# Kernel tuning notes

Hardware: AMD Instinct MI355X
Metric: run time of the kernel (lower is better)

The kernel has to match this reference:

```python
import jax, jax.numpy as jnp
import numpy as np

B, N, D, K, H = 64, 4096, 256, 11, 512
ITERS = 5
EPS = 1e-8
LN_EPS = 1e-5  # torch LayerNorm default
SCALE = D ** -0.5


def _ln(x, w, b):
    m = jnp.mean(x, axis=-1, keepdims=True)
    v = jnp.mean(jnp.square(x - m), axis=-1, keepdims=True)
    return (x - m) * jax.lax.rsqrt(v + LN_EPS) * w + b


def setup_inputs() -> dict:
    key = jax.random.key(0)
    ks = jax.random.split(key, 16)
    s = lambda k, shp, fan: jax.random.normal(k, shp, jnp.float32) * (1.0 / np.sqrt(fan))
    return {
        "inputs": jax.random.normal(ks[0], (B, N, D), jnp.float32),
        "slots_init": jax.random.normal(ks[1], (B, K, D), jnp.float32),
        "ln_f_w": jnp.ones((D,), jnp.float32), "ln_f_b": jnp.zeros((D,), jnp.float32),
        "ln_s_w": jnp.ones((D,), jnp.float32), "ln_s_b": jnp.zeros((D,), jnp.float32),
        "ln_p_w": jnp.ones((D,), jnp.float32), "ln_p_b": jnp.zeros((D,), jnp.float32),
        "Wq": s(ks[2], (D, D), D),
        "Wk": s(ks[3], (D, D), D),
        "Wv": s(ks[4], (D, D), D),
        "W_ih": s(ks[5], (3 * D, D), D), "b_ih": jnp.zeros((3 * D,), jnp.float32),
        "W_hh": s(ks[6], (3 * D, D), D), "b_hh": jnp.zeros((3 * D,), jnp.float32),
        "W1": s(ks[7], (H, D), D), "b1": jnp.zeros((H,), jnp.float32),
        "W2": s(ks[8], (D, H), H), "b2": jnp.zeros((D,), jnp.float32),
    }


def reference(inputs, slots_init, ln_f_w, ln_f_b, ln_s_w, ln_s_b, ln_p_w, ln_p_b,
              Wq, Wk, Wv, W_ih, b_ih, W_hh, b_hh, W1, b1, W2, b2):
    x = _ln(inputs, ln_f_w, ln_f_b)              # (B, N, D)
    k = x @ Wk.T                                  # (B, N, D)
    v = x @ Wv.T                                  # (B, N, D)
    slots = slots_init                            # (B, K, D)
    for _ in range(ITERS):
        slots_prev = slots
        q = _ln(slots, ln_s_w, ln_s_b) @ Wq.T     # (B, K, D)
        dots = jnp.einsum('bid,bjd->bij', q, k) * SCALE  # (B, K, N)
        attn = jax.nn.softmax(dots, axis=1) + EPS        # softmax over slots
        attn = attn / jnp.sum(attn, axis=-1, keepdims=True)
        updates = jnp.einsum('bjd,bij->bid', v, attn)    # (B, K, D)
        # GRUCell (torch semantics)
        gi = updates @ W_ih.T + b_ih              # (B, K, 3D)
        gh = slots_prev @ W_hh.T + b_hh
        i_r, i_z, i_n = jnp.split(gi, 3, axis=-1)
        h_r, h_z, h_n = jnp.split(gh, 3, axis=-1)
        r = jax.nn.sigmoid(i_r + h_r)
        z = jax.nn.sigmoid(i_z + h_z)
        n_ = jnp.tanh(i_n + r * h_n)
        slots = (1.0 - z) * n_ + z * slots_prev
        # residual MLP
        p = _ln(slots, ln_p_w, ln_p_b)
        slots = slots + jnp.maximum(p @ W1.T + b1, 0.0) @ W2.T + b2
    return slots
```

## Files before the change

kernel.cpp:

```cpp
#include <hip/hip_runtime.h>

typedef __bf16 bf16_t;
typedef bf16_t bf16x8 __attribute__((ext_vector_type(8)));
typedef bf16_t bf16x4 __attribute__((ext_vector_type(4)));
typedef float f32x4 __attribute__((ext_vector_type(4)));

#define DEVI static __device__ __forceinline__

constexpr int BB = 64;
constexpr int NN = 4096;
constexpr int DD = 256;
constexpr int KS = 11;
constexpr int KP = 16;
constexpr int HH = 512;
constexpr float EPS_A = 1e-8f;
constexpr float LNEPS = 1e-5f;
constexpr float SCALE = 0.0625f;
constexpr int MR = BB * KP;

DEVI float wredf(float v) {
#pragma unroll
  for (int o = 32; o > 0; o >>= 1) v += __shfl_xor(v, o, 64);
  return v;
}

DEVI float sigm(float x) { return 1.f / (1.f + __expf(-x)); }

__global__ void prep_weights_k(
    const float* __restrict__ s0, const float* __restrict__ s1, const float* __restrict__ s2,
    const float* __restrict__ s3, const float* __restrict__ s4, const float* __restrict__ s5,
    const float* __restrict__ s6,
    bf16_t* d0, bf16_t* d1, bf16_t* d2, bf16_t* d3, bf16_t* d4, bf16_t* d5, bf16_t* d6) {
  int i = blockIdx.x * 256 + threadIdx.x;
  const float* s; bf16_t* d; int o;
  if      (i < 65536)  { s = s0; d = d0; o = i; }
  else if (i < 131072) { s = s1; d = d1; o = i - 65536; }
  else if (i < 196608) { s = s2; d = d2; o = i - 131072; }
  else if (i < 393216) { s = s3; d = d3; o = i - 196608; }
  else if (i < 589824) { s = s4; d = d4; o = i - 393216; }
  else if (i < 720896) { s = s5; d = d5; o = i - 589824; }
  else                 { s = s6; d = d6; o = i - 720896; }
  d[o] = (bf16_t)s[o];
}

__global__ void init_slots_k(const float* __restrict__ si, float* __restrict__ slots) {
  int i = blockIdx.x * 256 + threadIdx.x;
  int d = i & 255, row = i >> 8, b = row >> 4, k = row & 15;
  slots[i] = (k < KS) ? si[((long)b * KS + k) * DD + d] : 0.f;
}

__global__ void ln_inputs_k(const float* __restrict__ x, const float* __restrict__ w,
                            const float* __restrict__ bsk, bf16_t* __restrict__ o) {
  const int wvi = threadIdx.x >> 6, lane = threadIdx.x & 63;
  const long row = (long)blockIdx.x * 4 + wvi;
  const float4 v = ((const float4*)(x + row * DD))[lane];
  float s = v.x + v.y + v.z + v.w;
  float s2 = v.x * v.x + v.y * v.y + v.z * v.z + v.w * v.w;
  s = wredf(s); s2 = wredf(s2);
  const float mean = s * (1.f / DD);
  const float var = s2 * (1.f / DD) - mean * mean;
  const float rstd = rsqrtf(var + LNEPS);
  const float4 w4 = ((const float4*)w)[lane];
  const float4 b4 = ((const float4*)bsk)[lane];
  bf16x4 ov;
  ov[0] = (bf16_t)((v.x - mean) * rstd * w4.x + b4.x);
  ov[1] = (bf16_t)((v.y - mean) * rstd * w4.y + b4.y);
  ov[2] = (bf16_t)((v.z - mean) * rstd * w4.z + b4.z);
  ov[3] = (bf16_t)((v.w - mean) * rstd * w4.w + b4.w);
  ((bf16x4*)(o + row * DD))[lane] = ov;
}

template <int MODE>
__global__ __launch_bounds__(256) void gemm_big_k(const bf16_t* __restrict__ X,
                                                  const bf16_t* __restrict__ W,
                                                  bf16_t* __restrict__ out) {
  __shared__ bf16_t As[128 * 72];
  __shared__ bf16_t Bs[256 * 72];
  const bf16_t* Ap; const bf16_t* Bp;
  if (MODE == 0) { Ap = W + (long)blockIdx.y * 128 * DD; Bp = X + (long)blockIdx.x * 256 * DD; }
  else           { Ap = X + (long)blockIdx.x * 128 * DD; Bp = W; }
  const int tid = threadIdx.x;
  const int wvi = tid >> 6, lane = tid & 63;
  const int c = lane & 15, q = lane >> 4;
  const int mh = wvi >> 1, nh = wvi & 1;
  f32x4 acc[4][8];
#pragma unroll
  for (int a = 0; a < 4; a++)
#pragma unroll
    for (int b = 0; b < 8; b++) acc[a][b] = (f32x4){0.f, 0.f, 0.f, 0.f};
  for (int kb = 0; kb < DD; kb += 64) {
#pragma unroll
    for (int it = 0; it < 4; ++it) {
      int id = it * 256 + tid, r = id >> 3, ch = id & 7;
      *(bf16x8*)(As + r * 72 + ch * 8) = *(const bf16x8*)(Ap + (long)r * DD + kb + ch * 8);
    }
#pragma unroll
    for (int it = 0; it < 8; ++it) {
      int id = it * 256 + tid, r = id >> 3, ch = id & 7;
      *(bf16x8*)(Bs + r * 72 + ch * 8) = *(const bf16x8*)(Bp + (long)r * DD + kb + ch * 8);
    }
    __syncthreads();
#pragma unroll
    for (int ks = 0; ks < 2; ++ks) {
      bf16x8 af[4], bfr[8];
#pragma unroll
      for (int mt = 0; mt < 4; mt++)
        af[mt] = *(const bf16x8*)(As + (mh * 64 + mt * 16 + c) * 72 + ks * 32 + q * 8);
#pragma unroll
      for (int nt = 0; nt < 8; nt++)
        bfr[nt] = *(const bf16x8*)(Bs + (nh * 128 + nt * 16 + c) * 72 + ks * 32 + q * 8);
#pragma unroll
      for (int mt = 0; mt < 4; mt++)
#pragma unroll
        for (int nt = 0; nt < 8; nt++)
          acc[mt][nt] = __builtin_amdgcn_mfma_f32_16x16x32_bf16(af[mt], bfr[nt], acc[mt][nt], 0, 0, 0);
    }
    __syncthreads();
  }
#pragma unroll
  for (int mt = 0; mt < 4; mt++) {
#pragma unroll
    for (int nt = 0; nt < 8; nt++) {
      bf16x4 o;
#pragma unroll
      for (int r = 0; r < 4; r++) o[r] = (bf16_t)acc[mt][nt][r];
      if (MODE == 0) {
        int dg = blockIdx.y * 128 + mh * 64 + mt * 16 + q * 4;
        long ng = (long)blockIdx.x * 256 + nh * 128 + nt * 16 + c;
        *(bf16x4*)(out + ng * DD + dg) = o;
      } else {
        long ng = (long)blockIdx.x * 128 + mh * 64 + mt * 16 + q * 4;
        int d = nh * 128 + nt * 16 + c;
        long b = ng >> 12; int nin = (int)(ng & 4095);
        *(bf16x4*)(out + (b * DD + d) * NN + nin) = o;
      }
    }
  }
}

__global__ void ln_slots_k(const float* __restrict__ slots, const float* __restrict__ lw,
                           const float* __restrict__ lb, bf16_t* __restrict__ sln,
                           bf16_t* __restrict__ spl, float* __restrict__ upd_raw,
                           float* __restrict__ rowsum) {
  const int row = blockIdx.x, d = threadIdx.x;
  upd_raw[row * DD + d] = 0.f;
  if (row < 4) rowsum[row * 256 + d] = 0.f;
  const int kk = row & 15;
  const int idx = row * DD + d;
  if (kk >= KS) { sln[idx] = (bf16_t)0.f; spl[idx] = (bf16_t)0.f; return; }
  float v = slots[idx];
  spl[idx] = (bf16_t)v;
  __shared__ float r1[4], r2[4];
  float s = wredf(v), s2 = wredf(v * v);
  const int wvi = threadIdx.x >> 6, lane = threadIdx.x & 63;
  if (lane == 0) { r1[wvi] = s; r2[wvi] = s2; }
  __syncthreads();
  float mean = (r1[0] + r1[1] + r1[2] + r1[3]) * (1.f / DD);
  float var = (r2[0] + r2[1] + r2[2] + r2[3]) * (1.f / DD) - mean * mean;
  float rstd = rsqrtf(var + LNEPS);
  sln[idx] = (bf16_t)((v - mean) * rstd * lw[d] + lb[d]);
}

template <bool BIASF, bool RELUF, bool RESF, int OUTM>
__global__ void small_gemm_k(const bf16_t* __restrict__ A, const bf16_t* __restrict__ W,
                             const float* __restrict__ bias, const float* __restrict__ res,
                             void* __restrict__ out, int C, int Kd) {
  const int lane = threadIdx.x & 63, c = lane & 15, q = lane >> 4;
  const int wid = blockIdx.x * 4 + (threadIdx.x >> 6);
  const int nct = C >> 4;
  const int mt = wid / nct, ct = wid % nct;
  const bf16_t* ap = A + (long)(mt * 16 + c) * Kd + q * 8;
  const bf16_t* wp = W + (long)(ct * 16 + c) * Kd + q * 8;
  f32x4 acc = (f32x4){0.f, 0.f, 0.f, 0.f};
  for (int k0 = 0; k0 < Kd; k0 += 32)
    acc = __builtin_amdgcn_mfma_f32_16x16x32_bf16(*(const bf16x8*)(ap + k0),
                                                  *(const bf16x8*)(wp + k0), acc, 0, 0, 0);
  const int col = ct * 16 + c;
  const float bv = BIASF ? bias[col] : 0.f;
#pragma unroll
  for (int r = 0; r < 4; r++) {
    const int row = mt * 16 + q * 4 + r;
    float v = acc[r] + bv;
    if (RELUF) v = fmaxf(v, 0.f);
    if (RESF) v += res[(long)row * C + col];
    if (OUTM == 0) ((float*)out)[(long)row * C + col] = v;
    else if (OUTM == 1) ((bf16_t*)out)[(long)row * C + col] = (bf16_t)v;
    else {
      int b = row >> 4, k2 = row & 15;
      if (k2 < KS) ((float*)out)[((long)b * KS + k2) * C + col] = v;
    }
  }
}

__global__ void dots_k(const bf16_t* __restrict__ qb, const bf16_t* __restrict__ kb,
                       float* __restrict__ dots) {
  const int b = blockIdx.x >> 3, strip = blockIdx.x & 7;
  const int wvi = threadIdx.x >> 6, lane = threadIdx.x & 63, c = lane & 15, q = lane >> 4;
  const int n0 = strip * 512 + wvi * 128;
  const bf16_t* qp = qb + (long)b * KP * DD;
  bf16x8 af[8];
#pragma unroll
  for (int kc = 0; kc < 8; kc++) af[kc] = *(const bf16x8*)(qp + c * DD + kc * 32 + q * 8);
  const bf16_t* kp = kb + (long)b * NN * DD;
  float* dp0 = dots + (long)b * KP * NN;
#pragma unroll
  for (int nt = 0; nt < 8; nt++) {
    f32x4 acc = (f32x4){0.f, 0.f, 0.f, 0.f};
    const bf16_t* bp = kp + (long)(n0 + nt * 16 + c) * DD + q * 8;
#pragma unroll
    for (int kc = 0; kc < 8; kc++)
      acc = __builtin_amdgcn_mfma_f32_16x16x32_bf16(af[kc], *(const bf16x8*)(bp + kc * 32), acc, 0, 0, 0);
    const int n = n0 + nt * 16 + c;
#pragma unroll
    for (int r = 0; r < 4; r++) dp0[(q * 4 + r) * NN + n] = acc[r] * SCALE;
  }
}

__global__ void softmax_k(const float* __restrict__ dots, bf16_t* __restrict__ att,
                          float* __restrict__ rowsum) {
  const int b = blockIdx.x >> 4, nc = blockIdx.x & 15;
  const int n = nc * 256 + threadIdx.x;
  const float* dp = dots + (long)b * KP * NN + n;
  float v[KS];
  float mx = -1e30f;
#pragma unroll
  for (int i = 0; i < KS; i++) { v[i] = dp[i * NN]; mx = fmaxf(mx, v[i]); }
  float sum = 0.f;
#pragma unroll
  for (int i = 0; i < KS; i++) { v[i] = __expf(v[i] - mx); sum += v[i]; }
  const float inv = 1.f / sum;
  bf16_t* ap = att + (long)b * KP * NN + n;
#pragma unroll
  for (int i = 0; i < KS; i++) { v[i] = v[i] * inv + EPS_A; ap[i * NN] = (bf16_t)v[i]; }
#pragma unroll
  for (int i = KS; i < KP; i++) ap[i * NN] = (bf16_t)0.f;
  __shared__ float red[KS][4];
  const int wvi = threadIdx.x >> 6, lane = threadIdx.x & 63;
#pragma unroll
  for (int i = 0; i < KS; i++) {
    float s = wredf(v[i]);
    if (lane == 0) red[i][wvi] = s;
  }
  __syncthreads();
  if (threadIdx.x < KS) {
    float s = red[threadIdx.x][0] + red[threadIdx.x][1] + red[threadIdx.x][2] + red[threadIdx.x][3];
    atomicAdd(&rowsum[b * KP + threadIdx.x], s);
  }
}

__global__ void updates_k(const bf16_t* __restrict__ att, const bf16_t* __restrict__ vT,
                          float* __restrict__ upd) {
  const int b = blockIdx.x >> 3, ksp = blockIdx.x & 7;
  const int wvi = threadIdx.x >> 6, lane = threadIdx.x & 63, c = lane & 15, q = lane >> 4;
  const int d0 = wvi * 64;
  const bf16_t* ab = att + (long)b * KP * NN;
  const bf16_t* vb = vT + (long)b * DD * NN;
  f32x4 acc[4];
#pragma unroll
  for (int dt = 0; dt < 4; dt++) acc[dt] = (f32x4){0.f, 0.f, 0.f, 0.f};
  const int j0b = ksp * 512;
  for (int j0 = j0b; j0 < j0b + 512; j0 += 32) {
    bf16x8 a = *(const bf16x8*)(ab + c * NN + j0 + q * 8);
#pragma unroll
    for (int dt = 0; dt < 4; dt++) {
      bf16x8 bb = *(const bf16x8*)(vb + (long)(d0 + dt * 16 + c) * NN + j0 + q * 8);
      acc[dt] = __builtin_amdgcn_mfma_f32_16x16x32_bf16(a, bb, acc[dt], 0, 0, 0);
    }
  }
  float* ub = upd + (long)b * KP * DD;
#pragma unroll
  for (int dt = 0; dt < 4; dt++)
#pragma unroll
    for (int r = 0; r < 4; r++)
      atomicAdd(&ub[(q * 4 + r) * DD + d0 + dt * 16 + c], acc[dt][r]);
}

__global__ void finalize_k(const float* __restrict__ upd, const float* __restrict__ rowsum,
                           bf16_t* __restrict__ o) {
  const int i = blockIdx.x * 256 + threadIdx.x;
  const int row = i >> 8, kk = row & 15;
  float v = 0.f;
  if (kk < KS) v = upd[i] / rowsum[row];
  o[i] = (bf16_t)v;
}

__global__ void gru_ln_k(const float* __restrict__ gi, const float* __restrict__ gh,
                         const float* __restrict__ sin_, const float* __restrict__ lw,
                         const float* __restrict__ lb, float* __restrict__ sout,
                         bf16_t* __restrict__ pbf) {
  const int row = blockIdx.x, d = threadIdx.x;
  const int kk = row & 15;
  const int idx = row * DD + d;
  if (kk >= KS) { sout[idx] = 0.f; pbf[idx] = (bf16_t)0.f; return; }
  const long g = (long)row * 768;
  float r = sigm(gi[g + d] + gh[g + d]);
  float z = sigm(gi[g + 256 + d] + gh[g + 256 + d]);
  float nn = tanhf(gi[g + 512 + d] + r * gh[g + 512 + d]);
  float sp = sin_[idx];
  float s = (1.f - z) * nn + z * sp;
  sout[idx] = s;
  __shared__ float r1[4], r2[4];
  float su = wredf(s), sq = wredf(s * s);
  const int wvi = threadIdx.x >> 6, lane = threadIdx.x & 63;
  if (lane == 0) { r1[wvi] = su; r2[wvi] = sq; }
  __syncthreads();
  float mean = (r1[0] + r1[1] + r1[2] + r1[3]) * (1.f / DD);
  float var = (r2[0] + r2[1] + r2[2] + r2[3]) * (1.f / DD) - mean * mean;
  float rstd = rsqrtf(var + LNEPS);
  pbf[idx] = (bf16_t)((s - mean) * rstd * lw[d] + lb[d]);
}

extern "C" void kernel_launch(void* const* d_in, const int* in_sizes, int n_in, void* d_out,
                              int out_size, void* d_ws, size_t ws_size, hipStream_t stream) {
  (void)in_sizes; (void)n_in; (void)out_size; (void)ws_size;
  const float* inputs = (const float*)d_in[0];
  const float* slots_in = (const float*)d_in[1];
  const float* ln_f_w = (const float*)d_in[2];
  const float* ln_f_b = (const float*)d_in[3];
  const float* ln_s_w = (const float*)d_in[4];
  const float* ln_s_b = (const float*)d_in[5];
  const float* ln_p_w = (const float*)d_in[6];
  const float* ln_p_b = (const float*)d_in[7];
  const float* Wq = (const float*)d_in[8];
  const float* Wk = (const float*)d_in[9];
  const float* Wv = (const float*)d_in[10];
  const float* W_ih = (const float*)d_in[11];
  const float* b_ih = (const float*)d_in[12];
  const float* W_hh = (const float*)d_in[13];
  const float* b_hh = (const float*)d_in[14];
  const float* W1 = (const float*)d_in[15];
  const float* b1 = (const float*)d_in[16];
  const float* W2 = (const float*)d_in[17];
  const float* b2 = (const float*)d_in[18];

  char* p = (char*)d_ws;
  auto alloc = [&](size_t bytes) { char* r = p; p += (bytes + 255) & ~(size_t)255; return r; };
  bf16_t* x_bf  = (bf16_t*)alloc((size_t)BB * NN * DD * 2);
  bf16_t* k_bf  = (bf16_t*)alloc((size_t)BB * NN * DD * 2);
  bf16_t* vT_bf = (bf16_t*)alloc((size_t)BB * NN * DD * 2);
  bf16_t* Wq_bf = (bf16_t*)alloc(65536 * 2);
  bf16_t* Wk_bf = (bf16_t*)alloc(65536 * 2);
  bf16_t* Wv_bf = (bf16_t*)alloc(65536 * 2);
  bf16_t* Wih_bf = (bf16_t*)alloc(196608 * 2);
  bf16_t* Whh_bf = (bf16_t*)alloc(196608 * 2);
  bf16_t* W1_bf = (bf16_t*)alloc(131072 * 2);
  bf16_t* W2_bf = (bf16_t*)alloc(131072 * 2);
  float* slots = (float*)alloc((size_t)MR * DD * 4);
  bf16_t* sln = (bf16_t*)alloc((size_t)MR * DD * 2);
  bf16_t* spl = (bf16_t*)alloc((size_t)MR * DD * 2);
  bf16_t* q_bf = (bf16_t*)alloc((size_t)MR * DD * 2);
  float* dots = (float*)alloc((size_t)BB * KP * NN * 4);
  bf16_t* att = (bf16_t*)alloc((size_t)BB * KP * NN * 2);
  float* rowsum = (float*)alloc((size_t)MR * 4);
  float* upd_raw = (float*)alloc((size_t)MR * DD * 4);
  bf16_t* upd_bf = (bf16_t*)alloc((size_t)MR * DD * 2);
  float* gi = (float*)alloc((size_t)MR * 768 * 4);
  float* gh = (float*)alloc((size_t)MR * 768 * 4);
  bf16_t* pbf = (bf16_t*)alloc((size_t)MR * DD * 2);
  bf16_t* h1 = (bf16_t*)alloc((size_t)MR * HH * 2);

  prep_weights_k<<<3328, 256, 0, stream>>>(Wq, Wk, Wv, W_ih, W_hh, W1, W2, Wq_bf, Wk_bf, Wv_bf,
                                           Wih_bf, Whh_bf, W1_bf, W2_bf);
  init_slots_k<<<1024, 256, 0, stream>>>(slots_in, slots);
  ln_inputs_k<<<65536, 256, 0, stream>>>(inputs, ln_f_w, ln_f_b, x_bf);
  gemm_big_k<0><<<dim3(1024, 2), 256, 0, stream>>>(x_bf, Wk_bf, k_bf);
  gemm_big_k<1><<<dim3(2048, 1), 256, 0, stream>>>(x_bf, Wv_bf, vT_bf);

  for (int t = 0; t < 5; t++) {
    ln_slots_k<<<1024, 256, 0, stream>>>(slots, ln_s_w, ln_s_b, sln, spl, upd_raw, rowsum);
    small_gemm_k<false, false, false, 1><<<256, 256, 0, stream>>>(sln, Wq_bf, nullptr, nullptr, q_bf, 256, 256);
    dots_k<<<512, 256, 0, stream>>>(q_bf, k_bf, dots);
    softmax_k<<<1024, 256, 0, stream>>>(dots, att, rowsum);
    updates_k<<<512, 256, 0, stream>>>(att, vT_bf, upd_raw);
    finalize_k<<<1024, 256, 0, stream>>>(upd_raw, rowsum, upd_bf);
    small_gemm_k<true, false, false, 0><<<768, 256, 0, stream>>>(upd_bf, Wih_bf, b_ih, nullptr, gi, 768, 256);
    small_gemm_k<true, false, false, 0><<<768, 256, 0, stream>>>(spl, Whh_bf, b_hh, nullptr, gh, 768, 256);
    gru_ln_k<<<1024, 256, 0, stream>>>(gi, gh, slots, ln_p_w, ln_p_b, slots, pbf);
    small_gemm_k<true, true, false, 1><<<512, 256, 0, stream>>>(pbf, W1_bf, b1, nullptr, h1, 512, 256);
    if (t < 4)
      small_gemm_k<true, false, true, 0><<<256, 256, 0, stream>>>(h1, W2_bf, b2, slots, slots, 256, 512);
    else
      small_gemm_k<true, false, true, 2><<<256, 256, 0, stream>>>(h1, W2_bf, b2, slots, d_out, 256, 512);
  }
}
```

Before: 1.198 ms.

## Fold Wk/Wv projections into slot-side weights and fuse per-iteration slot work

Drops the big K and V projections over all B*N tokens. It precomputes GW = scale*Wk^T Wq and Wihv = W_ih Wv, so attention and updates work directly on the layer-normed inputs and their transpose. Softmax is fused into the dots kernel, and LN-slots, q, finalize, GRU, LN and MLP are merged into one per-batch iter kernel. This removes two large GEMMs, the fp32 dots buffer and many small launches, at the cost of low-parallelism 64-block iteration kernels and bf16 rounding of the composed weights.

```diff
diff --git a/kernel.cpp b/kernel.cpp
--- a/kernel.cpp
+++ b/kernel.cpp
@@ -17,30 +17,36 @@
 constexpr float LNEPS = 1e-5f;
 constexpr float SCALE = 0.0625f;
 constexpr int MR = BB * KP;
-
-DEVI float wredf(float v) {
-#pragma unroll
-  for (int o = 32; o > 0; o >>= 1) v += __shfl_xor(v, o, 64);
-  return v;
-}
+constexpr int LDA = 264;
+constexpr int LDH = 520;
 
 DEVI float sigm(float x) { return 1.f / (1.f + __expf(-x)); }
 
-__global__ void prep_weights_k(
-    const float* __restrict__ s0, const float* __restrict__ s1, const float* __restrict__ s2,
-    const float* __restrict__ s3, const float* __restrict__ s4, const float* __restrict__ s5,
-    const float* __restrict__ s6,
-    bf16_t* d0, bf16_t* d1, bf16_t* d2, bf16_t* d3, bf16_t* d4, bf16_t* d5, bf16_t* d6) {
+__global__ void conv3_k(const float* __restrict__ a, const float* __restrict__ b,
+                        const float* __restrict__ c2,
+                        bf16_t* da, bf16_t* db, bf16_t* dc) {
   int i = blockIdx.x * 256 + threadIdx.x;
   const float* s; bf16_t* d; int o;
-  if      (i < 65536)  { s = s0; d = d0; o = i; }
-  else if (i < 131072) { s = s1; d = d1; o = i - 65536; }
-  else if (i < 196608) { s = s2; d = d2; o = i - 131072; }
-  else if (i < 393216) { s = s3; d = d3; o = i - 196608; }
-  else if (i < 589824) { s = s4; d = d4; o = i - 393216; }
-  else if (i < 720896) { s = s5; d = d5; o = i - 589824; }
-  else                 { s = s6; d = d6; o = i - 720896; }
+  if      (i < 196608) { s = a;  d = da; o = i; }
+  else if (i < 327680) { s = b;  d = db; o = i - 196608; }
+  else                 { s = c2; d = dc; o = i - 327680; }
   d[o] = (bf16_t)s[o];
+}
+
+__global__ void gw_k(const float* __restrict__ Wq, const float* __restrict__ Wk,
+                     bf16_t* __restrict__ GW) {
+  const int cc = blockIdx.x, e = threadIdx.x;
+  float acc = 0.f;
+  for (int d = 0; d < 256; d++) acc = fmaf(Wk[d * 256 + cc], Wq[d * 256 + e], acc);
+  GW[cc * 256 + e] = (bf16_t)(acc * SCALE);
+}
+
+__global__ void wihv_k(const float* __restrict__ Wih, const float* __restrict__ Wv,
+                       bf16_t* __restrict__ Wihv) {
+  const int cc = blockIdx.x, e = threadIdx.x;
+  float acc = 0.f;
+  for (int d = 0; d < 256; d++) acc = fmaf(Wih[cc * 256 + d], Wv[d * 256 + e], acc);
+  Wihv[cc * 256 + e] = (bf16_t)acc;
 }
 
 __global__ void init_slots_k(const float* __restrict__ si, float* __restrict__ slots) {
@@ -49,212 +55,117 @@
   slots[i] = (k < KS) ? si[((long)b * KS + k) * DD + d] : 0.f;
 }
 
-__global__ void ln_inputs_k(const float* __restrict__ x, const float* __restrict__ w,
-                            const float* __restrict__ bsk, bf16_t* __restrict__ o) {
-  const int wvi = threadIdx.x >> 6, lane = threadIdx.x & 63;
-  const long row = (long)blockIdx.x * 4 + wvi;
-  const float4 v = ((const float4*)(x + row * DD))[lane];
-  float s = v.x + v.y + v.z + v.w;
-  float s2 = v.x * v.x + v.y * v.y + v.z * v.z + v.w * v.w;
-  s = wredf(s); s2 = wredf(s2);
+__global__ __launch_bounds__(256) void ln_tr_k(const float* __restrict__ x,
+                                               const float* __restrict__ w,
+                                               const float* __restrict__ bsk,
+                                               bf16_t* __restrict__ xo,
+                                               bf16_t* __restrict__ xto) {
+  __shared__ bf16_t ts[32 * LDA];
+  const int b = blockIdx.x >> 7, nt = blockIdx.x & 127;
+  const int tid = threadIdx.x, g = tid >> 3, h = tid & 7;
+  const long row = (long)b * NN + nt * 32 + g;
+  const float4* src = (const float4*)(x + row * DD) + h * 8;
+  float4 v[8];
+  float s = 0.f, s2 = 0.f;
+#pragma unroll
+  for (int j = 0; j < 8; j++) {
+    v[j] = src[j];
+    s += v[j].x + v[j].y + v[j].z + v[j].w;
+    s2 += v[j].x * v[j].x + v[j].y * v[j].y + v[j].z * v[j].z + v[j].w * v[j].w;
+  }
+#pragma unroll
+  for (int off = 1; off < 8; off <<= 1) { s += __shfl_xor(s, off); s2 += __shfl_xor(s2, off); }
   const float mean = s * (1.f / DD);
   const float var = s2 * (1.f / DD) - mean * mean;
   const float rstd = rsqrtf(var + LNEPS);
-  const float4 w4 = ((const float4*)w)[lane];
-  const float4 b4 = ((const float4*)bsk)[lane];
-  bf16x4 ov;
-  ov[0] = (bf16_t)((v.x - mean) * rstd * w4.x + b4.x);
-  ov[1] = (bf16_t)((v.y - mean) * rstd * w4.y + b4.y);
-  ov[2] = (bf16_t)((v.z - mean) * rstd * w4.z + b4.z);
-  ov[3] = (bf16_t)((v.w - mean) * rstd * w4.w + b4.w);
-  ((bf16x4*)(o + row * DD))[lane] = ov;
-}
-
-template <int MODE>
-__global__ __launch_bounds__(256) void gemm_big_k(const bf16_t* __restrict__ X,
-                                                  const bf16_t* __restrict__ W,
-                                                  bf16_t* __restrict__ out) {
-  __shared__ bf16_t As[128 * 72];
-  __shared__ bf16_t Bs[256 * 72];
-  const bf16_t* Ap; const bf16_t* Bp;
-  if (MODE == 0) { Ap = W + (long)blockIdx.y * 128 * DD; Bp = X + (long)blockIdx.x * 256 * DD; }
-  else           { Ap = X + (long)blockIdx.x * 128 * DD; Bp = W; }
-  const int tid = threadIdx.x;
-  const int wvi = tid >> 6, lane = tid & 63;
-  const int c = lane & 15, q = lane >> 4;
-  const int mh = wvi >> 1, nh = wvi & 1;
-  f32x4 acc[4][8];
-#pragma unroll
-  for (int a = 0; a < 4; a++)
-#pragma unroll
-    for (int b = 0; b < 8; b++) acc[a][b] = (f32x4){0.f, 0.f, 0.f, 0.f};
-  for (int kb = 0; kb < DD; kb += 64) {
-#pragma unroll
-    for (int it = 0; it < 4; ++it) {
-      int id = it * 256 + tid, r = id >> 3, ch = id & 7;
-      *(bf16x8*)(As + r * 72 + ch * 8) = *(const bf16x8*)(Ap + (long)r * DD + kb + ch * 8);
-    }
-#pragma unroll
-    for (int it = 0; it < 8; ++it) {
-      int id = it * 256 + tid, r = id >> 3, ch = id & 7;
-      *(bf16x8*)(Bs + r * 72 + ch * 8) = *(const bf16x8*)(Bp + (long)r * DD + kb + ch * 8);
-    }
-    __syncthreads();
-#pragma unroll
-    for (int ks = 0; ks < 2; ++ks) {
-      bf16x8 af[4], bfr[8];
-#pragma unroll
-      for (int mt = 0; mt < 4; mt++)
-        af[mt] = *(const bf16x8*)(As + (mh * 64 + mt * 16 + c) * 72 + ks * 32 + q * 8);
-#pragma unroll
-      for (int nt = 0; nt < 8; nt++)
-        bfr[nt] = *(const bf16x8*)(Bs + (nh * 128 + nt * 16 + c) * 72 + ks * 32 + q * 8);
-#pragma unroll
-      for (int mt = 0; mt < 4; mt++)
-#pragma unroll
-        for (int nt = 0; nt < 8; nt++)
-          acc[mt][nt] = __builtin_amdgcn_mfma_f32_16x16x32_bf16(af[mt], bfr[nt], acc[mt][nt], 0, 0, 0);
-    }
-    __syncthreads();
-  }
-#pragma unroll
-  for (int mt = 0; mt < 4; mt++) {
-#pragma unroll
-    for (int nt = 0; nt < 8; nt++) {
-      bf16x4 o;
-#pragma unroll
-      for (int r = 0; r < 4; r++) o[r] = (bf16_t)acc[mt][nt][r];
-      if (MODE == 0) {
-        int dg = blockIdx.y * 128 + mh * 64 + mt * 16 + q * 4;
-        long ng = (long)blockIdx.x * 256 + nh * 128 + nt * 16 + c;
-        *(bf16x4*)(out + ng * DD + dg) = o;
-      } else {
-        long ng = (long)blockIdx.x * 128 + mh * 64 + mt * 16 + q * 4;
-        int d = nh * 128 + nt * 16 + c;
-        long b = ng >> 12; int nin = (int)(ng & 4095);
-        *(bf16x4*)(out + (b * DD + d) * NN + nin) = o;
-      }
-    }
-  }
-}
-
-__global__ void ln_slots_k(const float* __restrict__ slots, const float* __restrict__ lw,
-                           const float* __restrict__ lb, bf16_t* __restrict__ sln,
-                           bf16_t* __restrict__ spl, float* __restrict__ upd_raw,
-                           float* __restrict__ rowsum) {
-  const int row = blockIdx.x, d = threadIdx.x;
-  upd_raw[row * DD + d] = 0.f;
-  if (row < 4) rowsum[row * 256 + d] = 0.f;
-  const int kk = row & 15;
-  const int idx = row * DD + d;
-  if (kk >= KS) { sln[idx] = (bf16_t)0.f; spl[idx] = (bf16_t)0.f; return; }
-  float v = slots[idx];
-  spl[idx] = (bf16_t)v;
-  __shared__ float r1[4], r2[4];
-  float s = wredf(v), s2 = wredf(v * v);
-  const int wvi = threadIdx.x >> 6, lane = threadIdx.x & 63;
-  if (lane == 0) { r1[wvi] = s; r2[wvi] = s2; }
+  const float4* w4 = (const float4*)w + h * 8;
+  const float4* b4 = (const float4*)bsk + h * 8;
+  bf16x8* xrow = (bf16x8*)(xo + row * DD) + h * 4;
+#pragma unroll
+  for (int j2 = 0; j2 < 4; j2++) {
+    float4 a0 = v[2 * j2], a1 = v[2 * j2 + 1];
+    float4 w0 = w4[2 * j2], w1 = w4[2 * j2 + 1];
+    float4 bb0 = b4[2 * j2], bb1 = b4[2 * j2 + 1];
+    bf16x8 o;
+    o[0] = (bf16_t)((a0.x - mean) * rstd * w0.x + bb0.x);
+    o[1] = (bf16_t)((a0.y - mean) * rstd * w0.y + bb0.y);
+    o[2] = (bf16_t)((a0.z - mean) * rstd * w0.z + bb0.z);
+    o[3] = (bf16_t)((a0.w - mean) * rstd * w0.w + bb0.w);
+    o[4] = (bf16_t)((a1.x - mean) * rstd * w1.x + bb1.x);
+    o[5] = (bf16_t)((a1.y - mean) * rstd * w1.y + bb1.y);
+    o[6] = (bf16_t)((a1.z - mean) * rstd * w1.z + bb1.z);
+    o[7] = (bf16_t)((a1.w - mean) * rstd * w1.w + bb1.w);
+    xrow[j2] = o;
+    *(bf16x8*)(ts + g * LDA + h * 32 + j2 * 8) = o;
+  }
   __syncthreads();
-  float mean = (r1[0] + r1[1] + r1[2] + r1[3]) * (1.f / DD);
-  float var = (r2[0] + r2[1] + r2[2] + r2[3]) * (1.f / DD) - mean * mean;
-  float rstd = rsqrtf(var + LNEPS);
-  sln[idx] = (bf16_t)((v - mean) * rstd * lw[d] + lb[d]);
-}
-
-template <bool BIASF, bool RELUF, bool RESF, int OUTM>
-__global__ void small_gemm_k(const bf16_t* __restrict__ A, const bf16_t* __restrict__ W,
-                             const float* __restrict__ bias, const float* __restrict__ res,
-                             void* __restrict__ out, int C, int Kd) {
-  const int lane = threadIdx.x & 63, c = lane & 15, q = lane >> 4;
-  const int wid = blockIdx.x * 4 + (threadIdx.x >> 6);
-  const int nct = C >> 4;
-  const int mt = wid / nct, ct = wid % nct;
-  const bf16_t* ap = A + (long)(mt * 16 + c) * Kd + q * 8;
-  const bf16_t* wp = W + (long)(ct * 16 + c) * Kd + q * 8;
-  f32x4 acc = (f32x4){0.f, 0.f, 0.f, 0.f};
-  for (int k0 = 0; k0 < Kd; k0 += 32)
-    acc = __builtin_amdgcn_mfma_f32_16x16x32_bf16(*(const bf16x8*)(ap + k0),
-                                                  *(const bf16x8*)(wp + k0), acc, 0, 0, 0);
-  const int col = ct * 16 + c;
-  const float bv = BIASF ? bias[col] : 0.f;
-#pragma unroll
-  for (int r = 0; r < 4; r++) {
-    const int row = mt * 16 + q * 4 + r;
-    float v = acc[r] + bv;
-    if (RELUF) v = fmaxf(v, 0.f);
-    if (RESF) v += res[(long)row * C + col];
-    if (OUTM == 0) ((float*)out)[(long)row * C + col] = v;
-    else if (OUTM == 1) ((bf16_t*)out)[(long)row * C + col] = (bf16_t)v;
-    else {
-      int b = row >> 4, k2 = row & 15;
-      if (k2 < KS) ((float*)out)[((long)b * KS + k2) * C + col] = v;
-    }
-  }
-}
-
-__global__ void dots_k(const bf16_t* __restrict__ qb, const bf16_t* __restrict__ kb,
-                       float* __restrict__ dots) {
+#pragma unroll
+  for (int p = 0; p < 4; p++) {
+    const int e = p * 64 + (tid >> 2), nc = (tid & 3) * 8;
+    bf16x8 o2;
+#pragma unroll
+    for (int j = 0; j < 8; j++) o2[j] = ts[(nc + j) * LDA + e];
+    *(bf16x8*)(xto + ((long)b * DD + e) * NN + nt * 32 + nc) = o2;
+  }
+}
+
+__global__ __launch_bounds__(256) void attn1_k(const bf16_t* __restrict__ q2,
+                                               const bf16_t* __restrict__ xb,
+                                               bf16_t* __restrict__ att,
+                                               float* __restrict__ rowsum) {
   const int b = blockIdx.x >> 3, strip = blockIdx.x & 7;
-  const int wvi = threadIdx.x >> 6, lane = threadIdx.x & 63, c = lane & 15, q = lane >> 4;
-  const int n0 = strip * 512 + wvi * 128;
-  const bf16_t* qp = qb + (long)b * KP * DD;
+  const int wv = threadIdx.x >> 6, lane = threadIdx.x & 63, c = lane & 15, qq = lane >> 4;
+  const int n0 = strip * 512 + wv * 128;
+  const bf16_t* qp = q2 + (long)b * KP * DD;
   bf16x8 af[8];
 #pragma unroll
-  for (int kc = 0; kc < 8; kc++) af[kc] = *(const bf16x8*)(qp + c * DD + kc * 32 + q * 8);
-  const bf16_t* kp = kb + (long)b * NN * DD;
-  float* dp0 = dots + (long)b * KP * NN;
+  for (int kc = 0; kc < 8; kc++) af[kc] = *(const bf16x8*)(qp + c * DD + kc * 32 + qq * 8);
+  const bf16_t* xp = xb + (long)b * NN * DD;
+  bf16_t* ap = att + (long)b * KP * NN;
+  float rs[4] = {0.f, 0.f, 0.f, 0.f};
 #pragma unroll
   for (int nt = 0; nt < 8; nt++) {
     f32x4 acc = (f32x4){0.f, 0.f, 0.f, 0.f};
-    const bf16_t* bp = kp + (long)(n0 + nt * 16 + c) * DD + q * 8;
+    const bf16_t* bp = xp + (long)(n0 + nt * 16 + c) * DD + qq * 8;
 #pragma unroll
     for (int kc = 0; kc < 8; kc++)
       acc = __builtin_amdgcn_mfma_f32_16x16x32_bf16(af[kc], *(const bf16x8*)(bp + kc * 32), acc, 0, 0, 0);
+    float mx = -1e30f;
+#pragma unroll
+    for (int r = 0; r < 4; r++) if (qq * 4 + r < KS) mx = fmaxf(mx, acc[r]);
+    mx = fmaxf(mx, __shfl_xor(mx, 16)); mx = fmaxf(mx, __shfl_xor(mx, 32));
+    float ev[4], sum = 0.f;
+#pragma unroll
+    for (int r = 0; r < 4; r++) { ev[r] = (qq * 4 + r < KS) ? __expf(acc[r] - mx) : 0.f; sum += ev[r]; }
+    sum += __shfl_xor(sum, 16); sum += __shfl_xor(sum, 32);
+    const float inv = 1.f / sum;
     const int n = n0 + nt * 16 + c;
 #pragma unroll
-    for (int r = 0; r < 4; r++) dp0[(q * 4 + r) * NN + n] = acc[r] * SCALE;
-  }
-}
-
-__global__ void softmax_k(const float* __restrict__ dots, bf16_t* __restrict__ att,
-                          float* __restrict__ rowsum) {
-  const int b = blockIdx.x >> 4, nc = blockIdx.x & 15;
-  const int n = nc * 256 + threadIdx.x;
-  const float* dp = dots + (long)b * KP * NN + n;
-  float v[KS];
-  float mx = -1e30f;
-#pragma unroll
-  for (int i = 0; i < KS; i++) { v[i] = dp[i * NN]; mx = fmaxf(mx, v[i]); }
-  float sum = 0.f;
-#pragma unroll
-  for (int i = 0; i < KS; i++) { v[i] = __expf(v[i] - mx); sum += v[i]; }
-  const float inv = 1.f / sum;
-  bf16_t* ap = att + (long)b * KP * NN + n;
-#pragma unroll
-  for (int i = 0; i < KS; i++) { v[i] = v[i] * inv + EPS_A; ap[i * NN] = (bf16_t)v[i]; }
-#pragma unroll
-  for (int i = KS; i < KP; i++) ap[i * NN] = (bf16_t)0.f;
-  __shared__ float red[KS][4];
-  const int wvi = threadIdx.x >> 6, lane = threadIdx.x & 63;
-#pragma unroll
-  for (int i = 0; i < KS; i++) {
-    float s = wredf(v[i]);
-    if (lane == 0) red[i][wvi] = s;
-  }
-  __syncthreads();
-  if (threadIdx.x < KS) {
-    float s = red[threadIdx.x][0] + red[threadIdx.x][1] + red[threadIdx.x][2] + red[threadIdx.x][3];
-    atomicAdd(&rowsum[b * KP + threadIdx.x], s);
-  }
-}
-
-__global__ void updates_k(const bf16_t* __restrict__ att, const bf16_t* __restrict__ vT,
+    for (int r = 0; r < 4; r++) {
+      float a = (qq * 4 + r < KS) ? ev[r] * inv + EPS_A : 0.f;
+      rs[r] += a;
+      ap[(qq * 4 + r) * NN + n] = (bf16_t)a;
+    }
+  }
+#pragma unroll
+  for (int r = 0; r < 4; r++) {
+#pragma unroll
+    for (int off = 8; off >= 1; off >>= 1) rs[r] += __shfl_xor(rs[r], off);
+  }
+  if (c == 0) {
+#pragma unroll
+    for (int r = 0; r < 4; r++)
+      if (qq * 4 + r < KS) atomicAdd(&rowsum[b * KP + qq * 4 + r], rs[r]);
+  }
+}
+
+__global__ void updates_k(const bf16_t* __restrict__ att, const bf16_t* __restrict__ xT,
                           float* __restrict__ upd) {
   const int b = blockIdx.x >> 3, ksp = blockIdx.x & 7;
   const int wvi = threadIdx.x >> 6, lane = threadIdx.x & 63, c = lane & 15, q = lane >> 4;
   const int d0 = wvi * 64;
   const bf16_t* ab = att + (long)b * KP * NN;
-  const bf16_t* vb = vT + (long)b * DD * NN;
+  const bf16_t* vb = xT + (long)b * DD * NN;
   f32x4 acc[4];
 #pragma unroll
   for (int dt = 0; dt < 4; dt++) acc[dt] = (f32x4){0.f, 0.f, 0.f, 0.f};
@@ -275,39 +186,197 @@
       atomicAdd(&ub[(q * 4 + r) * DD + d0 + dt * 16 + c], acc[dt][r]);
 }
 
-__global__ void finalize_k(const float* __restrict__ upd, const float* __restrict__ rowsum,
-                           bf16_t* __restrict__ o) {
-  const int i = blockIdx.x * 256 + threadIdx.x;
-  const int row = i >> 8, kk = row & 15;
-  float v = 0.f;
-  if (kk < KS) v = upd[i] / rowsum[row];
-  o[i] = (bf16_t)v;
-}
-
-__global__ void gru_ln_k(const float* __restrict__ gi, const float* __restrict__ gh,
-                         const float* __restrict__ sin_, const float* __restrict__ lw,
-                         const float* __restrict__ lb, float* __restrict__ sout,
-                         bf16_t* __restrict__ pbf) {
-  const int row = blockIdx.x, d = threadIdx.x;
-  const int kk = row & 15;
-  const int idx = row * DD + d;
-  if (kk >= KS) { sout[idx] = 0.f; pbf[idx] = (bf16_t)0.f; return; }
-  const long g = (long)row * 768;
-  float r = sigm(gi[g + d] + gh[g + d]);
-  float z = sigm(gi[g + 256 + d] + gh[g + 256 + d]);
-  float nn = tanhf(gi[g + 512 + d] + r * gh[g + 512 + d]);
-  float sp = sin_[idx];
-  float s = (1.f - z) * nn + z * sp;
-  sout[idx] = s;
-  __shared__ float r1[4], r2[4];
-  float su = wredf(s), sq = wredf(s * s);
-  const int wvi = threadIdx.x >> 6, lane = threadIdx.x & 63;
-  if (lane == 0) { r1[wvi] = su; r2[wvi] = sq; }
+DEVI void row_ln(float (&v)[4][4], const float* __restrict__ lw, const float* __restrict__ lb,
+                 bf16_t* dst, float (*red)[4][16], int w, int c, int qq, int E0) {
+  float ps[4], pq[4];
+#pragma unroll
+  for (int r = 0; r < 4; r++) {
+    ps[r] = v[0][r] + v[1][r] + v[2][r] + v[3][r];
+    pq[r] = v[0][r] * v[0][r] + v[1][r] * v[1][r] + v[2][r] * v[2][r] + v[3][r] * v[3][r];
+  }
+#pragma unroll
+  for (int r = 0; r < 4; r++) {
+#pragma unroll
+    for (int off = 1; off < 16; off <<= 1) {
+      ps[r] += __shfl_xor(ps[r], off);
+      pq[r] += __shfl_xor(pq[r], off);
+    }
+  }
+  if (c == 0) {
+#pragma unroll
+    for (int r = 0; r < 4; r++) { red[0][w][qq * 4 + r] = ps[r]; red[1][w][qq * 4 + r] = pq[r]; }
+  }
   __syncthreads();
-  float mean = (r1[0] + r1[1] + r1[2] + r1[3]) * (1.f / DD);
-  float var = (r2[0] + r2[1] + r2[2] + r2[3]) * (1.f / DD) - mean * mean;
-  float rstd = rsqrtf(var + LNEPS);
-  pbf[idx] = (bf16_t)((s - mean) * rstd * lw[d] + lb[d]);
+#pragma unroll
+  for (int r = 0; r < 4; r++) {
+    const int R = qq * 4 + r;
+    const float m = (red[0][0][R] + red[0][1][R] + red[0][2][R] + red[0][3][R]) * (1.f / DD);
+    const float va = (red[1][0][R] + red[1][1][R] + red[1][2][R] + red[1][3][R]) * (1.f / DD) - m * m;
+    const float rstd = rsqrtf(va + LNEPS);
+#pragma unroll
+    for (int et = 0; et < 4; et++) {
+      const int col = E0 + et * 16 + c;
+      dst[R * LDA + col] = (bf16_t)((v[et][r] - m) * rstd * lw[col] + lb[col]);
+    }
+  }
+  __syncthreads();
+}
+
+template <int PHASE>
+__global__ __launch_bounds__(256, 1) void iter_k(
+    float* __restrict__ updR, float* __restrict__ rowsum, float* __restrict__ slots,
+    const float* __restrict__ b_ih, const float* __restrict__ b_hh,
+    const bf16_t* __restrict__ Wihv, const bf16_t* __restrict__ Whh,
+    const bf16_t* __restrict__ W1, const float* __restrict__ b1,
+    const bf16_t* __restrict__ W2, const float* __restrict__ b2,
+    const float* __restrict__ lpw, const float* __restrict__ lpb,
+    const float* __restrict__ lsw, const float* __restrict__ lsb,
+    const bf16_t* __restrict__ GW, bf16_t* __restrict__ q2,
+    float* __restrict__ dout, int last) {
+  __shared__ bf16_t uN[16 * LDA];
+  __shared__ bf16_t sS[16 * LDA];
+  __shared__ bf16_t pS[16 * LDA];
+  __shared__ bf16_t h1S[16 * LDH];
+  __shared__ float red[2][4][16];
+  const int b = blockIdx.x;
+  const int tid = threadIdx.x, w = tid >> 6, lane = tid & 63, c = lane & 15, qq = lane >> 4;
+  const int E0 = w * 64;
+  const long base = (long)b * 16 * 256;
+  float sf[4][4];
+
+  if (PHASE == 1) {
+    float rsv[4];
+#pragma unroll
+    for (int r = 0; r < 4; r++) rsv[r] = rowsum[b * 16 + qq * 4 + r];
+    float sp[4][4];
+#pragma unroll
+    for (int et = 0; et < 4; et++) {
+#pragma unroll
+      for (int r = 0; r < 4; r++) {
+        const int R = qq * 4 + r, col = E0 + et * 16 + c;
+        const long gidx = base + (long)R * 256 + col;
+        float u = updR[gidx]; updR[gidx] = 0.f;
+        float sv = slots[gidx];
+        sp[et][r] = sv;
+        float un = (R < KS) ? u / rsv[r] : 0.f;
+        uN[R * LDA + col] = (bf16_t)un;
+        sS[R * LDA + col] = (bf16_t)sv;
+      }
+    }
+    __syncthreads();
+    bf16x8 afu[8], afs[8];
+#pragma unroll
+    for (int kc = 0; kc < 8; kc++) {
+      afu[kc] = *(const bf16x8*)(uN + c * LDA + kc * 32 + qq * 8);
+      afs[kc] = *(const bf16x8*)(sS + c * LDA + kc * 32 + qq * 8);
+    }
+    float rg[4][4], zg[4][4];
+#pragma unroll
+    for (int g = 0; g < 3; g++) {
+      f32x4 ai[4], ah[4];
+#pragma unroll
+      for (int et = 0; et < 4; et++) { ai[et] = (f32x4){0,0,0,0}; ah[et] = (f32x4){0,0,0,0}; }
+#pragma unroll
+      for (int et = 0; et < 4; et++) {
+        const bf16_t* wi = Wihv + ((long)(g * 256 + E0 + et * 16 + c)) * 256 + qq * 8;
+        const bf16_t* wh = Whh + ((long)(g * 256 + E0 + et * 16 + c)) * 256 + qq * 8;
+#pragma unroll
+        for (int kc = 0; kc < 8; kc++) {
+          ai[et] = __builtin_amdgcn_mfma_f32_16x16x32_bf16(afu[kc], *(const bf16x8*)(wi + kc * 32), ai[et], 0, 0, 0);
+          ah[et] = __builtin_amdgcn_mfma_f32_16x16x32_bf16(afs[kc], *(const bf16x8*)(wh + kc * 32), ah[et], 0, 0, 0);
+        }
+      }
+#pragma unroll
+      for (int et = 0; et < 4; et++) {
+        const int col = E0 + et * 16 + c;
+        const float bi = b_ih[g * 256 + col], bh = b_hh[g * 256 + col];
+#pragma unroll
+        for (int r = 0; r < 4; r++) {
+          const float xi = ai[et][r] + bi, xh = ah[et][r] + bh;
+          if (g == 0) rg[et][r] = sigm(xi + xh);
+          else if (g == 1) zg[et][r] = sigm(xi + xh);
+          else {
+            const float nh = tanhf(xi + rg[et][r] * xh);
+            sf[et][r] = (1.f - zg[et][r]) * nh + zg[et][r] * sp[et][r];
+          }
+        }
+      }
+    }
+    row_ln(sf, lpw, lpb, pS, red, w, c, qq, E0);
+    bf16x8 afp[8];
+#pragma unroll
+    for (int kc = 0; kc < 8; kc++) afp[kc] = *(const bf16x8*)(pS + c * LDA + kc * 32 + qq * 8);
+#pragma unroll
+    for (int ht = 0; ht < 8; ht++) {
+      f32x4 a0 = (f32x4){0, 0, 0, 0};
+      const int colh = w * 128 + ht * 16 + c;
+      const bf16_t* w1p = W1 + (long)colh * 256 + qq * 8;
+#pragma unroll
+      for (int kc = 0; kc < 8; kc++)
+        a0 = __builtin_amdgcn_mfma_f32_16x16x32_bf16(afp[kc], *(const bf16x8*)(w1p + kc * 32), a0, 0, 0, 0);
+      const float bv = b1[colh];
+#pragma unroll
+      for (int r = 0; r < 4; r++) h1S[(qq * 4 + r) * LDH + colh] = (bf16_t)fmaxf(a0[r] + bv, 0.f);
+    }
+    __syncthreads();
+    f32x4 ao[4];
+#pragma unroll
+    for (int et = 0; et < 4; et++) ao[et] = (f32x4){0, 0, 0, 0};
+#pragma unroll
+    for (int kc2 = 0; kc2 < 16; kc2++) {
+      const bf16x8 afh = *(const bf16x8*)(h1S + c * LDH + kc2 * 32 + qq * 8);
+#pragma unroll
+      for (int et = 0; et < 4; et++)
+        ao[et] = __builtin_amdgcn_mfma_f32_16x16x32_bf16(
+            afh, *(const bf16x8*)(W2 + (long)(E0 + et * 16 + c) * 512 + kc2 * 32 + qq * 8), ao[et], 0, 0, 0);
+    }
+#pragma unroll
+    for (int et = 0; et < 4; et++)
+#pragma unroll
+      for (int r = 0; r < 4; r++)
+        sf[et][r] = ao[et][r] + b2[E0 + et * 16 + c] + sf[et][r];
+    if (last) {
+#pragma unroll
+      for (int et = 0; et < 4; et++)
+#pragma unroll
+        for (int r = 0; r < 4; r++) {
+          const int R = qq * 4 + r;
+          if (R < KS) dout[((long)b * KS + R) * 256 + E0 + et * 16 + c] = sf[et][r];
+        }
+      return;
+    }
+#pragma unroll
+    for (int et = 0; et < 4; et++)
+#pragma unroll
+      for (int r = 0; r < 4; r++)
+        slots[base + (long)(qq * 4 + r) * 256 + E0 + et * 16 + c] = sf[et][r];
+  } else {
+#pragma unroll
+    for (int et = 0; et < 4; et++) {
+#pragma unroll
+      for (int r = 0; r < 4; r++) {
+        const long gidx = base + (long)(qq * 4 + r) * 256 + E0 + et * 16 + c;
+        sf[et][r] = slots[gidx];
+        updR[gidx] = 0.f;
+      }
+    }
+  }
+  row_ln(sf, lsw, lsb, pS, red, w, c, qq, E0);
+  bf16x8 afq[8];
+#pragma unroll
+  for (int kc = 0; kc < 8; kc++) afq[kc] = *(const bf16x8*)(pS + c * LDA + kc * 32 + qq * 8);
+#pragma unroll
+  for (int et = 0; et < 4; et++) {
+    f32x4 aq = (f32x4){0, 0, 0, 0};
+    const bf16_t* gp = GW + (long)(E0 + et * 16 + c) * 256 + qq * 8;
+#pragma unroll
+    for (int kc = 0; kc < 8; kc++)
+      aq = __builtin_amdgcn_mfma_f32_16x16x32_bf16(afq[kc], *(const bf16x8*)(gp + kc * 32), aq, 0, 0, 0);
+#pragma unroll
+    for (int r = 0; r < 4; r++)
+      q2[base + (long)(qq * 4 + r) * 256 + E0 + et * 16 + c] = (bf16_t)aq[r];
+  }
+  if (tid < 16) rowsum[b * 16 + tid] = 0.f;
 }
 
 extern "C" void kernel_launch(void* const* d_in, const int* in_sizes, int n_in, void* d_out,
@@ -335,51 +404,32 @@
 
   char* p = (char*)d_ws;
   auto alloc = [&](size_t bytes) { char* r = p; p += (bytes + 255) & ~(size_t)255; return r; };
-  bf16_t* x_bf  = (bf16_t*)alloc((size_t)BB * NN * DD * 2);
-  bf16_t* k_bf  = (bf16_t*)alloc((size_t)BB * NN * DD * 2);
-  bf16_t* vT_bf = (bf16_t*)alloc((size_t)BB * NN * DD * 2);
-  bf16_t* Wq_bf = (bf16_t*)alloc(65536 * 2);
-  bf16_t* Wk_bf = (bf16_t*)alloc(65536 * 2);
-  bf16_t* Wv_bf = (bf16_t*)alloc(65536 * 2);
-  bf16_t* Wih_bf = (bf16_t*)alloc(196608 * 2);
+  bf16_t* x_bf   = (bf16_t*)alloc((size_t)BB * NN * DD * 2);
+  bf16_t* xT_bf  = (bf16_t*)alloc((size_t)BB * NN * DD * 2);
+  bf16_t* GW_bf  = (bf16_t*)alloc(65536 * 2);
+  bf16_t* Wihv_bf = (bf16_t*)alloc(196608 * 2);
   bf16_t* Whh_bf = (bf16_t*)alloc(196608 * 2);
-  bf16_t* W1_bf = (bf16_t*)alloc(131072 * 2);
-  bf16_t* W2_bf = (bf16_t*)alloc(131072 * 2);
-  float* slots = (float*)alloc((size_t)MR * DD * 4);
-  bf16_t* sln = (bf16_t*)alloc((size_t)MR * DD * 2);
-  bf16_t* spl = (bf16_t*)alloc((size_t)MR * DD * 2);
-  bf16_t* q_bf = (bf16_t*)alloc((size_t)MR * DD * 2);
-  float* dots = (float*)alloc((size_t)BB * KP * NN * 4);
-  bf16_t* att = (bf16_t*)alloc((size_t)BB * KP * NN * 2);
-  float* rowsum = (float*)alloc((size_t)MR * 4);
-  float* upd_raw = (float*)alloc((size_t)MR * DD * 4);
-  bf16_t* upd_bf = (bf16_t*)alloc((size_t)MR * DD * 2);
-  float* gi = (float*)alloc((size_t)MR * 768 * 4);
-  float* gh = (float*)alloc((size_t)MR * 768 * 4);
-  bf16_t* pbf = (bf16_t*)alloc((size_t)MR * DD * 2);
-  bf16_t* h1 = (bf16_t*)alloc((size_t)MR * HH * 2);
-
-  prep_weights_k<<<3328, 256, 0, stream>>>(Wq, Wk, Wv, W_ih, W_hh, W1, W2, Wq_bf, Wk_bf, Wv_bf,
-                                           Wih_bf, Whh_bf, W1_bf, W2_bf);
+  bf16_t* W1_bf  = (bf16_t*)alloc(131072 * 2);
+  bf16_t* W2_bf  = (bf16_t*)alloc(131072 * 2);
+  float* slots   = (float*)alloc((size_t)MR * DD * 4);
+  bf16_t* q2_bf  = (bf16_t*)alloc((size_t)MR * DD * 2);
+  bf16_t* att    = (bf16_t*)alloc((size_t)BB * KP * NN * 2);
+  float* updR    = (float*)alloc((size_t)MR * DD * 4);
+  float* rowsum  = (float*)alloc((size_t)MR * 4);
+
+  conv3_k<<<1792, 256, 0, stream>>>(W_hh, W1, W2, Whh_bf, W1_bf, W2_bf);
+  gw_k<<<256, 256, 0, stream>>>(Wq, Wk, GW_bf);
+  wihv_k<<<768, 256, 0, stream>>>(W_ih, Wv, Wihv_bf);
   init_slots_k<<<1024, 256, 0, stream>>>(slots_in, slots);
-  ln_inputs_k<<<65536, 256, 0, stream>>>(inputs, ln_f_w, ln_f_b, x_bf);
-  gemm_big_k<0><<<dim3(1024, 2), 256, 0, stream>>>(x_bf, Wk_bf, k_bf);
-  gemm_big_k<1><<<dim3(2048, 1), 256, 0, stream>>>(x_bf, Wv_bf, vT_bf);
-
+  ln_tr_k<<<8192, 256, 0, stream>>>(inputs, ln_f_w, ln_f_b, x_bf, xT_bf);
+  iter_k<0><<<64, 256, 0, stream>>>(updR, rowsum, slots, b_ih, b_hh, Wihv_bf, Whh_bf,
+                                    W1_bf, b1, W2_bf, b2, ln_p_w, ln_p_b, ln_s_w, ln_s_b,
+                                    GW_bf, q2_bf, nullptr, 0);
   for (int t = 0; t < 5; t++) {
-    ln_slots_k<<<1024, 256, 0, stream>>>(slots, ln_s_w, ln_s_b, sln, spl, upd_raw, rowsum);
-    small_gemm_k<false, false, false, 1><<<256, 256, 0, stream>>>(sln, Wq_bf, nullptr, nullptr, q_bf, 256, 256);
-    dots_k<<<512, 256, 0, stream>>>(q_bf, k_bf, dots);
-    softmax_k<<<1024, 256, 0, stream>>>(dots, att, rowsum);
-    updates_k<<<512, 256, 0, stream>>>(att, vT_bf, upd_raw);
-    finalize_k<<<1024, 256, 0, stream>>>(upd_raw, rowsum, upd_bf);
-    small_gemm_k<true, false, false, 0><<<768, 256, 0, stream>>>(upd_bf, Wih_bf, b_ih, nullptr, gi, 768, 256);
-    small_gemm_k<true, false, false, 0><<<768, 256, 0, stream>>>(spl, Whh_bf, b_hh, nullptr, gh, 768, 256);
-    gru_ln_k<<<1024, 256, 0, stream>>>(gi, gh, slots, ln_p_w, ln_p_b, slots, pbf);
-    small_gemm_k<true, true, false, 1><<<512, 256, 0, stream>>>(pbf, W1_bf, b1, nullptr, h1, 512, 256);
-    if (t < 4)
-      small_gemm_k<true, false, true, 0><<<256, 256, 0, stream>>>(h1, W2_bf, b2, slots, slots, 256, 512);
-    else
-      small_gemm_k<true, false, true, 2><<<256, 256, 0, stream>>>(h1, W2_bf, b2, slots, d_out, 256, 512);
-  }
-}
+    attn1_k<<<512, 256, 0, stream>>>(q2_bf, x_bf, att, rowsum);
+    updates_k<<<512, 256, 0, stream>>>(att, xT_bf, updR);
+    iter_k<1><<<64, 256, 0, stream>>>(updR, rowsum, slots, b_ih, b_hh, Wihv_bf, Whh_bf,
+                                      W1_bf, b1, W2_bf, b2, ln_p_w, ln_p_b, ln_s_w, ln_s_b,
+                                      GW_bf, q2_bf, (float*)d_out, t == 4);
+  }
+}
```

Result: faster. 1.126 ms (-6.0%).
